# Optimization experiments

Measured on AMD Instinct MI355X. Metric: run time of the kernel, lower is better.

The kernel has to match this reference:

```python
import jax, jax.numpy as jnp
import numpy as np

N_NODES = 100_000
N_EDGES = 1_200_000
N_GRAPHS = 512
HID = 64


def setup_inputs() -> dict:
    key = jax.random.key(0)
    ks = jax.random.split(key, 8)
    x = jax.random.normal(ks[0], (N_NODES, 2), dtype=jnp.float32)
    edge_index = jax.random.randint(ks[1], (2, N_EDGES), 0, N_NODES, dtype=jnp.int32)
    batch = jnp.sort(jax.random.randint(ks[2], (N_NODES,), 0, N_GRAPHS, dtype=jnp.int32))
    def glorot(k, shape):
        fan_in, fan_out = shape
        s = jnp.sqrt(6.0 / (fan_in + fan_out))
        return jax.random.uniform(k, shape, jnp.float32, -s, s)
    return {
        "x": x, "edge_index": edge_index, "batch": batch, "num_graphs": N_GRAPHS,
        "W1": glorot(ks[3], (2, HID)), "b1": jnp.zeros((HID,), jnp.float32),
        "W2": glorot(ks[4], (HID, HID)), "b2": jnp.zeros((HID,), jnp.float32),
        "Wf1": glorot(ks[5], (HID, HID)), "bf1": jnp.zeros((HID,), jnp.float32),
        "Wf2": glorot(ks[6], (HID, 4)), "bf2": jnp.zeros((4,), jnp.float32),
    }


def gcn_conv(x, W, b, src, dst, n_nodes):
    """PyG GCNConv: sym-normalized A with self-loops, then linear."""
    h = x @ W  # [N, H] transform first (as PyG does)
    ones = jnp.ones(src.shape[0], x.dtype)
    deg = jax.ops.segment_sum(ones, dst, num_segments=n_nodes) + 1.0  # +1 self-loop
    dinv = jax.lax.rsqrt(deg)  # deg >= 1 always
    norm = dinv[src] * dinv[dst]  # [E]
    agg = jax.ops.segment_sum(h[src] * norm[:, None], dst, num_segments=n_nodes)
    agg = agg + h * (dinv * dinv)[:, None]  # self-loop contribution
    return agg + b


def global_mean_pool(x, batch, num_graphs):
    sums = jax.ops.segment_sum(x, batch, num_segments=num_graphs)
    cnts = jax.ops.segment_sum(jnp.ones(x.shape[0], x.dtype), batch, num_segments=num_graphs)
    return sums / jnp.maximum(cnts, 1.0)[:, None]


def reference(x, edge_index, batch, num_graphs, W1, b1, W2, b2, Wf1, bf1, Wf2, bf2):
    n = x.shape[0]
    src, dst = edge_index[0], edge_index[1]
    h = jax.nn.relu(gcn_conv(x, W1, b1, src, dst, n))   # dropout = identity (eval)
    h = jax.nn.relu(gcn_conv(h, W2, b2, src, dst, n))
    g = global_mean_pool(h, batch, num_graphs)          # [num_graphs, HID]
    g = jax.nn.relu(g @ Wf1 + bf1)
    return g @ Wf2 + bf2                                # [num_graphs, 4]
```

## Files before the change

### kernel.cpp

```cpp
#include <hip/hip_runtime.h>
#include <hip/hip_fp16.h>

#define NG 512
#define HID 64
#define CSH 9
#define BKT (1 << CSH)
#define PTILE 4096
#define MAXB 1024

__device__ __forceinline__ int pad8(int d) { return (d + 7) & ~7; }

__global__ __launch_bounds__(256) void partA_kernel(
    const int* __restrict__ src, const int* __restrict__ dst,
    const int* __restrict__ batch, int* __restrict__ gstart,
    int* __restrict__ bcnt, int* __restrict__ pstage,
    int E, int N, int nbc, int S) {
    __shared__ int hist[MAXB];
    __shared__ int base[MAXB];
    int tid = threadIdx.x;
    int t0 = blockIdx.x * PTILE;
    for (int i = blockIdx.x * 256 + tid; i < N; i += gridDim.x * 256) {
        int b = batch[i];
        int bp = (i == 0) ? -1 : batch[i - 1];
        for (int g = bp + 1; g <= b; ++g) gstart[g] = i;
        if (i == N - 1)
            for (int g = b + 1; g <= NG; ++g) gstart[g] = N;
    }
    for (int i = tid; i < nbc; i += 256) hist[i] = 0;
    __syncthreads();
    int es[PTILE / 256], ds[PTILE / 256];
#pragma unroll
    for (int j = 0; j < PTILE / 256; ++j) {
        int e = t0 + j * 256 + tid;
        if (e < E) {
            ds[j] = dst[e];
            es[j] = src[e];
            atomicAdd(&hist[ds[j] >> CSH], 1);
        } else {
            ds[j] = -1;
        }
    }
    __syncthreads();
    for (int i = tid; i < nbc; i += 256) {
        int c = hist[i];
        base[i] = c ? atomicAdd(&bcnt[i], c) : 0;
        hist[i] = 0;
    }
    __syncthreads();
#pragma unroll
    for (int j = 0; j < PTILE / 256; ++j) {
        if (ds[j] >= 0) {
            int b = ds[j] >> CSH;
            int r = base[b] + atomicAdd(&hist[b], 1);
            if (r < S)
                pstage[(size_t)b * S + r] = (es[j] << CSH) | (ds[j] & (BKT - 1));
        }
    }
}

__global__ __launch_bounds__(256) void partB2_kernel(
    const int* __restrict__ pstage, const int* __restrict__ bcnt,
    const float2* __restrict__ x2, int* __restrict__ deg, float* __restrict__ dinv,
    float2* __restrict__ xs2, int* __restrict__ rowbeg, int* __restrict__ esrc,
    int* __restrict__ ecur, int N, int S) {
    __shared__ int h[BKT];
    __shared__ int rowL[BKT];
    __shared__ int curL[BKT];
    __shared__ int ps[256];
    __shared__ int baseS;
    int c = blockIdx.x;
    int n0 = c << CSH;
    int tid = threadIdx.x;
    for (int i = tid; i < BKT; i += 256) h[i] = 0;
    __syncthreads();
    int cnt = min(bcnt[c], S);
    const int* pst = pstage + (size_t)c * S;
    for (int i = tid; i < cnt; i += 256) atomicAdd(&h[pst[i] & (BKT - 1)], 1);
    __syncthreads();
    int i0 = 2 * tid, i1 = 2 * tid + 1;
    int dg0 = (n0 + i0 < N) ? h[i0] : 0;
    int dg1 = (n0 + i1 < N) ? h[i1] : 0;
    if (n0 + i0 < N) {
        deg[n0 + i0] = dg0;
        float di = rsqrtf((float)dg0 + 1.0f);
        dinv[n0 + i0] = di;
        float2 xv = x2[n0 + i0];
        xs2[n0 + i0] = make_float2(xv.x * di, xv.y * di);
    }
    if (n0 + i1 < N) {
        deg[n0 + i1] = dg1;
        float di = rsqrtf((float)dg1 + 1.0f);
        dinv[n0 + i1] = di;
        float2 xv = x2[n0 + i1];
        xs2[n0 + i1] = make_float2(xv.x * di, xv.y * di);
    }
    int p0 = pad8(dg0), p1 = pad8(dg1);
    ps[tid] = p0 + p1;
    __syncthreads();
    for (int off = 1; off < 256; off <<= 1) {
        int t = (tid >= off) ? ps[tid - off] : 0;
        __syncthreads();
        ps[tid] += t;
        __syncthreads();
    }
    if (tid == 255) baseS = atomicAdd(ecur, ps[255]);
    __syncthreads();
    int excl = baseS + ps[tid] - (p0 + p1);
    rowL[i0] = excl;
    rowL[i1] = excl + p0;
    curL[i0] = 0;
    curL[i1] = 0;
    if (n0 + i0 < N) rowbeg[n0 + i0] = rowL[i0];
    if (n0 + i1 < N) rowbeg[n0 + i1] = rowL[i1];
    __syncthreads();
    for (int i = tid; i < cnt; i += 256) {
        int w = pst[i];
        int l = w & (BKT - 1);
        int p = rowL[l] + atomicAdd(&curL[l], 1);
        esrc[p] = w >> CSH;
    }
    __syncthreads();
    for (int l = tid; l < BKT; l += 256) {
        if (n0 + l < N) {
            int dg = curL[l];
            int p = rowL[l] + dg, p1e = rowL[l] + pad8(dg);
            for (; p < p1e; ++p) esrc[p] = N;
        }
    }
    if (c == 0 && tid == 0) xs2[N] = make_float2(0.0f, 0.0f);
}

__global__ __launch_bounds__(256) void layer1a_kernel(
    const float2* __restrict__ xs2, const int* __restrict__ rowbeg,
    const int* __restrict__ deg, const int* __restrict__ esrc,
    const float* __restrict__ dinv, const float* __restrict__ W1,
    const float* __restrict__ b1, float* __restrict__ h1s, int N) {
    int t = blockIdx.x * blockDim.x + threadIdx.x;
    int node = t >> 6, lane = t & 63;
    if (node >= N) return;
    int un = __builtin_amdgcn_readfirstlane(node);
    int k0 = __builtin_amdgcn_readfirstlane(rowbeg[un]);
    int k1 = k0 + pad8(__builtin_amdgcn_readfirstlane(deg[un]));
    float a0 = 0.0f, a1 = 0.0f;
    for (int e = k0; e < k1; e += 8) {
        const int4* ep = (const int4*)(esrc + e);
        int4 qa = ep[0], qb = ep[1];
        float2 v0 = xs2[qa.x], v1 = xs2[qa.y], v2 = xs2[qa.z], v3 = xs2[qa.w];
        float2 v4 = xs2[qb.x], v5 = xs2[qb.y], v6 = xs2[qb.z], v7 = xs2[qb.w];
        a0 += ((v0.x + v1.x) + (v2.x + v3.x)) + ((v4.x + v5.x) + (v6.x + v7.x));
        a1 += ((v0.y + v1.y) + (v2.y + v3.y)) + ((v4.y + v5.y) + (v6.y + v7.y));
    }
    float di = dinv[un];
    float2 xn = xs2[un];
    float m0 = di * (a0 + xn.x);
    float m1 = di * (a1 + xn.y);
    float v = fmaf(m0, W1[lane], fmaf(m1, W1[HID + lane], b1[lane]));
    h1s[(size_t)un * HID + lane] = fmaxf(v, 0.0f) * di;
}

#define TNB 128
__global__ __launch_bounds__(TNB) void l1gemm_kernel(
    const float* __restrict__ h1s, const float* __restrict__ W2,
    __half* __restrict__ h2, int N) {
    __shared__ float h1t[HID * TNB];
    int t = threadIdx.x;
    int node0 = blockIdx.x * TNB;
    const float4* g4 = (const float4*)h1s;
#pragma unroll
    for (int r = 0; r < 16; ++r) {
        int g = r * TNB + t;
        int nd = g >> 4, kq = g & 15;
        float4 v = make_float4(0.f, 0.f, 0.f, 0.f);
        if (node0 + nd < N) v = g4[(size_t)(node0 + nd) * 16 + kq];
        int kb = kq * 4;
        h1t[(kb + 0) * TNB + (nd ^ ((kb + 0) & 31))] = v.x;
        h1t[(kb + 1) * TNB + (nd ^ ((kb + 1) & 31))] = v.y;
        h1t[(kb + 2) * TNB + (nd ^ ((kb + 2) & 31))] = v.z;
        h1t[(kb + 3) * TNB + (nd ^ ((kb + 3) & 31))] = v.w;
    }
    __syncthreads();
    int node = node0 + t;
    bool alive = node < N;
#pragma unroll 1
    for (int jt = 0; jt < 8; ++jt) {
        float c0 = 0.f, c1 = 0.f, c2 = 0.f, c3 = 0.f;
        float c4 = 0.f, c5 = 0.f, c6 = 0.f, c7 = 0.f;
#pragma unroll 8
        for (int k = 0; k < HID; ++k) {
            float h = h1t[k * TNB + (t ^ (k & 31))];
            const float4* wr = (const float4*)(W2 + k * HID + jt * 8);
            float4 wa = wr[0], wb = wr[1];
            c0 = fmaf(h, wa.x, c0); c1 = fmaf(h, wa.y, c1);
            c2 = fmaf(h, wa.z, c2); c3 = fmaf(h, wa.w, c3);
            c4 = fmaf(h, wb.x, c4); c5 = fmaf(h, wb.y, c5);
            c6 = fmaf(h, wb.z, c6); c7 = fmaf(h, wb.w, c7);
        }
        if (alive) {
            union { __half h[8]; int4 v; } u;
            u.h[0] = __float2half_rn(c0); u.h[1] = __float2half_rn(c1);
            u.h[2] = __float2half_rn(c2); u.h[3] = __float2half_rn(c3);
            u.h[4] = __float2half_rn(c4); u.h[5] = __float2half_rn(c5);
            u.h[6] = __float2half_rn(c6); u.h[7] = __float2half_rn(c7);
            *(int4*)(h2 + (size_t)node * HID + jt * 8) = u.v;
        }
    }
}

__global__ __launch_bounds__(256, 8) void layer2_kernel(
    const int* __restrict__ rowbeg, const int* __restrict__ deg,
    const int* __restrict__ esrc, const float* __restrict__ dinv,
    const __half* __restrict__ h2, const float* __restrict__ b2,
    const int* __restrict__ batch, float* __restrict__ gsum, int N) {
    int lane = threadIdx.x & 63;
    float bz = b2[lane];
    int wave = (blockIdx.x * 256 + threadIdx.x) >> 6;
    int nwaves = gridDim.x * 4;
    int npw = (N + nwaves - 1) / nwaves;
    int nA = wave * npw;
    int nB = min(N, nA + npw);
    int gcur = -1;
    float zacc = 0.0f;
    for (int node = nA; node < nB; ++node) {
        int un = __builtin_amdgcn_readfirstlane(node);
        int k0 = __builtin_amdgcn_readfirstlane(rowbeg[un]);
        int k1 = k0 + pad8(__builtin_amdgcn_readfirstlane(deg[un]));
        float acc = __half2float(h2[(un << 6) + lane]);
        int e = k0;
        for (; e + 32 <= k1; e += 32) {
            const int4* ep = (const int4*)(esrc + e);
            int4 q0 = ep[0], q1 = ep[1], q2 = ep[2], q3 = ep[3];
            int4 q4 = ep[4], q5 = ep[5], q6 = ep[6], q7 = ep[7];
            float r0  = __half2float(h2[(q0.x << 6) + lane]);
            float r1  = __half2float(h2[(q0.y << 6) + lane]);
            float r2  = __half2float(h2[(q0.z << 6) + lane]);
            float r3  = __half2float(h2[(q0.w << 6) + lane]);
            float r4  = __half2float(h2[(q1.x << 6) + lane]);
            float r5  = __half2float(h2[(q1.y << 6) + lane]);
            float r6  = __half2float(h2[(q1.z << 6) + lane]);
            float r7  = __half2float(h2[(q1.w << 6) + lane]);
            float r8  = __half2float(h2[(q2.x << 6) + lane]);
            float r9  = __half2float(h2[(q2.y << 6) + lane]);
            float r10 = __half2float(h2[(q2.z << 6) + lane]);
            float r11 = __half2float(h2[(q2.w << 6) + lane]);
            float r12 = __half2float(h2[(q3.x << 6) + lane]);
            float r13 = __half2float(h2[(q3.y << 6) + lane]);
            float r14 = __half2float(h2[(q3.z << 6) + lane]);
            float r15 = __half2float(h2[(q3.w << 6) + lane]);
            float r16 = __half2float(h2[(q4.x << 6) + lane]);
            float r17 = __half2float(h2[(q4.y << 6) + lane]);
            float r18 = __half2float(h2[(q4.z << 6) + lane]);
            float r19 = __half2float(h2[(q4.w << 6) + lane]);
            float r20 = __half2float(h2[(q5.x << 6) + lane]);
            float r21 = __half2float(h2[(q5.y << 6) + lane]);
            float r22 = __half2float(h2[(q5.z << 6) + lane]);
            float r23 = __half2float(h2[(q5.w << 6) + lane]);
            float r24 = __half2float(h2[(q6.x << 6) + lane]);
            float r25 = __half2float(h2[(q6.y << 6) + lane]);
            float r26 = __half2float(h2[(q6.z << 6) + lane]);
            float r27 = __half2float(h2[(q6.w << 6) + lane]);
            float r28 = __half2float(h2[(q7.x << 6) + lane]);
            float r29 = __half2float(h2[(q7.y << 6) + lane]);
            float r30 = __half2float(h2[(q7.z << 6) + lane]);
            float r31 = __half2float(h2[(q7.w << 6) + lane]);
            acc += ((((r0 + r1) + (r2 + r3)) + ((r4 + r5) + (r6 + r7)))
                  + (((r8 + r9) + (r10 + r11)) + ((r12 + r13) + (r14 + r15))))
                 + ((((r16 + r17) + (r18 + r19)) + ((r20 + r21) + (r22 + r23)))
                  + (((r24 + r25) + (r26 + r27)) + ((r28 + r29) + (r30 + r31))));
        }
        if (e + 16 <= k1) {
            const int4* ep = (const int4*)(esrc + e);
            int4 qa = ep[0], qb = ep[1], qc = ep[2], qd = ep[3];
            float r0 = __half2float(h2[(qa.x << 6) + lane]);
            float r1 = __half2float(h2[(qa.y << 6) + lane]);
            float r2 = __half2float(h2[(qa.z << 6) + lane]);
            float r3 = __half2float(h2[(qa.w << 6) + lane]);
            float r4 = __half2float(h2[(qb.x << 6) + lane]);
            float r5 = __half2float(h2[(qb.y << 6) + lane]);
            float r6 = __half2float(h2[(qb.z << 6) + lane]);
            float r7 = __half2float(h2[(qb.w << 6) + lane]);
            float r8 = __half2float(h2[(qc.x << 6) + lane]);
            float r9 = __half2float(h2[(qc.y << 6) + lane]);
            float r10 = __half2float(h2[(qc.z << 6) + lane]);
            float r11 = __half2float(h2[(qc.w << 6) + lane]);
            float r12 = __half2float(h2[(qd.x << 6) + lane]);
            float r13 = __half2float(h2[(qd.y << 6) + lane]);
            float r14 = __half2float(h2[(qd.z << 6) + lane]);
            float r15 = __half2float(h2[(qd.w << 6) + lane]);
            acc += (((r0 + r1) + (r2 + r3)) + ((r4 + r5) + (r6 + r7)))
                 + (((r8 + r9) + (r10 + r11)) + ((r12 + r13) + (r14 + r15)));
            e += 16;
        }
        if (e < k1) {
            const int4* ep = (const int4*)(esrc + e);
            int4 qa = ep[0], qb = ep[1];
            float r0 = __half2float(h2[(qa.x << 6) + lane]);
            float r1 = __half2float(h2[(qa.y << 6) + lane]);
            float r2 = __half2float(h2[(qa.z << 6) + lane]);
            float r3 = __half2float(h2[(qa.w << 6) + lane]);
            float r4 = __half2float(h2[(qb.x << 6) + lane]);
            float r5 = __half2float(h2[(qb.y << 6) + lane]);
            float r6 = __half2float(h2[(qb.z << 6) + lane]);
            float r7 = __half2float(h2[(qb.w << 6) + lane]);
            acc += ((r0 + r1) + (r2 + r3)) + ((r4 + r5) + (r6 + r7));
        }
        float z = fmaxf(fmaf(dinv[un], acc, bz), 0.0f);
        int g = __builtin_amdgcn_readfirstlane(batch[un]);
        if (g != gcur) {
            if (gcur >= 0) atomicAdd(&gsum[(gcur << 6) + lane], zacc);
            gcur = g;
            zacc = 0.0f;
        }
        zacc += z;
    }
    if (gcur >= 0) atomicAdd(&gsum[(gcur << 6) + lane], zacc);
}

__global__ void head_kernel(const float* __restrict__ gsum, const int* __restrict__ gstart,
                            const float* __restrict__ Wf1, const float* __restrict__ bf1,
                            const float* __restrict__ Wf2, const float* __restrict__ bf2,
                            float* __restrict__ out) {
    __shared__ float gs[HID];
    __shared__ float ts[HID];
    int b = blockIdx.x;
    int j = threadIdx.x;
    float cnt = fmaxf((float)(gstart[b + 1] - gstart[b]), 1.0f);
    gs[j] = gsum[b * HID + j] / cnt;
    __syncthreads();
    float acc = bf1[j];
#pragma unroll
    for (int k = 0; k < HID; ++k) acc = fmaf(gs[k], Wf1[k * HID + j], acc);
    ts[j] = fmaxf(acc, 0.0f);
    __syncthreads();
    if (j < 4) {
        float o = bf2[j];
#pragma unroll
        for (int k = 0; k < HID; ++k) o = fmaf(ts[k], Wf2[k * 4 + j], o);
        out[b * 4 + j] = o;
    }
}

extern "C" void kernel_launch(void* const* d_in, const int* in_sizes, int n_in,
                              void* d_out, int out_size, void* d_ws, size_t ws_size,
                              hipStream_t stream) {
    const float* x   = (const float*)d_in[0];
    const int*   ei  = (const int*)d_in[1];
    const int*   bat = (const int*)d_in[2];
    const float* W1  = (const float*)d_in[4];
    const float* b1  = (const float*)d_in[5];
    const float* W2  = (const float*)d_in[6];
    const float* b2  = (const float*)d_in[7];
    const float* Wf1 = (const float*)d_in[8];
    const float* bf1 = (const float*)d_in[9];
    const float* Wf2 = (const float*)d_in[10];
    const float* bf2 = (const float*)d_in[11];
    float* out = (float*)d_out;

    int N = in_sizes[2];
    int E = in_sizes[1] / 2;
    const int* src = ei;
    const int* dst = ei + E;
    int nbc = (N + BKT - 1) >> CSH;
    int ntile = (E + PTILE - 1) / PTILE;
    int S = 2 * (E / nbc) + 1024;
    size_t Ecap = ((size_t)E + 7 * (size_t)N + 8 + 3) & ~(size_t)3;

    char* ws = (char*)d_ws;
    size_t off = 0;
    auto alloc = [&](size_t bytes) {
        char* p = ws + off;
        off = (off + bytes + 255) & ~(size_t)255;
        return p;
    };
    int*    bcnt   = (int*)alloc((size_t)MAXB * 4);
    int*    ecur   = (int*)alloc(256);
    float*  gsum   = (float*)alloc((size_t)NG * HID * 4);
    int*    deg    = (int*)alloc((size_t)N * 4);
    float*  dinv   = (float*)alloc((size_t)N * 4);
    int*    rowbeg = (int*)alloc((size_t)N * 4);
    int*    esrc   = (int*)alloc(Ecap * 4);
    int*    pstage = (int*)alloc((size_t)nbc * S * 4);
    float2* xs2    = (float2*)alloc((size_t)(N + 1) * 8);
    float*  h1buf  = (float*)alloc((size_t)N * HID * 4);
    __half* h2buf  = (__half*)alloc((size_t)(N + 1) * HID * 2);
    int*    gstart = (int*)alloc((size_t)(NG + 1) * 4);

    hipMemsetAsync(bcnt, 0, (size_t)((char*)gsum - (char*)bcnt) + (size_t)NG * HID * 4,
                   stream);
    hipMemsetAsync(h2buf + (size_t)N * HID, 0, HID * 2, stream);

    partA_kernel<<<ntile, 256, 0, stream>>>(src, dst, bat, gstart, bcnt, pstage, E, N,
                                            nbc, S);
    partB2_kernel<<<nbc, 256, 0, stream>>>(pstage, bcnt, (const float2*)x, deg, dinv, xs2,
                                           rowbeg, esrc, ecur, N, S);

    int nh = N * HID;
    layer1a_kernel<<<(nh + 255) / 256, 256, 0, stream>>>(xs2, rowbeg, deg, esrc, dinv, W1,
                                                         b1, h1buf, N);
    l1gemm_kernel<<<(N + TNB - 1) / TNB, TNB, 0, stream>>>(h1buf, W2, h2buf, N);

    layer2_kernel<<<4096, 256, 0, stream>>>(rowbeg, deg, esrc, dinv, h2buf, b2, bat, gsum,
                                            N);

    head_kernel<<<NG, HID, 0, stream>>>(gsum, gstart, Wf1, bf1, Wf2, bf2, out);
}
```

Measured before the change: 225.9 us.

## Fuse layer-1 aggregation with W2 GEMM via shared-memory tile, drop h1 buffer

Merges the layer-1 aggregation kernel and the 64x64 GEMM kernel into one. Each block aggregates 64 nodes, writes the scaled hidden vectors straight into a swizzled shared tile, then four waves each compute two output column groups. This removes the float32 h1 round trip through global memory (about 25 MB written and read back) and one kernel launch. The zeroing of the padding row moves from a memset into partB2. In exchange, GEMM parallelism changes, since each block handles fewer nodes and splits columns across waves, and the gather phase runs with one node per wave sequentially.

```diff
diff --git a/kernel.cpp b/kernel.cpp
--- a/kernel.cpp
+++ b/kernel.cpp
@@ -7,6 +7,7 @@
 #define BKT (1 << CSH)
 #define PTILE 4096
 #define MAXB 1024
+#define TNB 64
 
 __device__ __forceinline__ int pad8(int d) { return (d + 7) & ~7; }
 
@@ -62,7 +63,7 @@
     const int* __restrict__ pstage, const int* __restrict__ bcnt,
     const float2* __restrict__ x2, int* __restrict__ deg, float* __restrict__ dinv,
     float2* __restrict__ xs2, int* __restrict__ rowbeg, int* __restrict__ esrc,
-    int* __restrict__ ecur, int N, int S) {
+    int* __restrict__ ecur, __half* __restrict__ h2, int N, int S) {
     __shared__ int h[BKT];
     __shared__ int rowL[BKT];
     __shared__ int curL[BKT];
@@ -127,67 +128,60 @@
             for (; p < p1e; ++p) esrc[p] = N;
         }
     }
-    if (c == 0 && tid == 0) xs2[N] = make_float2(0.0f, 0.0f);
-}
-
-__global__ __launch_bounds__(256) void layer1a_kernel(
+    if (c == 0) {
+        if (tid == 0) xs2[N] = make_float2(0.0f, 0.0f);
+        if (tid < 8)
+            ((int4*)(h2 + (size_t)N * HID))[tid] = make_int4(0, 0, 0, 0);
+    }
+}
+
+__global__ __launch_bounds__(256) void layer1f_kernel(
     const float2* __restrict__ xs2, const int* __restrict__ rowbeg,
     const int* __restrict__ deg, const int* __restrict__ esrc,
     const float* __restrict__ dinv, const float* __restrict__ W1,
-    const float* __restrict__ b1, float* __restrict__ h1s, int N) {
-    int t = blockIdx.x * blockDim.x + threadIdx.x;
-    int node = t >> 6, lane = t & 63;
-    if (node >= N) return;
-    int un = __builtin_amdgcn_readfirstlane(node);
-    int k0 = __builtin_amdgcn_readfirstlane(rowbeg[un]);
-    int k1 = k0 + pad8(__builtin_amdgcn_readfirstlane(deg[un]));
-    float a0 = 0.0f, a1 = 0.0f;
-    for (int e = k0; e < k1; e += 8) {
-        const int4* ep = (const int4*)(esrc + e);
-        int4 qa = ep[0], qb = ep[1];
-        float2 v0 = xs2[qa.x], v1 = xs2[qa.y], v2 = xs2[qa.z], v3 = xs2[qa.w];
-        float2 v4 = xs2[qb.x], v5 = xs2[qb.y], v6 = xs2[qb.z], v7 = xs2[qb.w];
-        a0 += ((v0.x + v1.x) + (v2.x + v3.x)) + ((v4.x + v5.x) + (v6.x + v7.x));
-        a1 += ((v0.y + v1.y) + (v2.y + v3.y)) + ((v4.y + v5.y) + (v6.y + v7.y));
-    }
-    float di = dinv[un];
-    float2 xn = xs2[un];
-    float m0 = di * (a0 + xn.x);
-    float m1 = di * (a1 + xn.y);
-    float v = fmaf(m0, W1[lane], fmaf(m1, W1[HID + lane], b1[lane]));
-    h1s[(size_t)un * HID + lane] = fmaxf(v, 0.0f) * di;
-}
-
-#define TNB 128
-__global__ __launch_bounds__(TNB) void l1gemm_kernel(
-    const float* __restrict__ h1s, const float* __restrict__ W2,
+    const float* __restrict__ b1, const float* __restrict__ W2,
     __half* __restrict__ h2, int N) {
     __shared__ float h1t[HID * TNB];
-    int t = threadIdx.x;
+    int tid = threadIdx.x;
+    int lane = tid & 63;
+    int wv = tid >> 6;
     int node0 = blockIdx.x * TNB;
-    const float4* g4 = (const float4*)h1s;
-#pragma unroll
-    for (int r = 0; r < 16; ++r) {
-        int g = r * TNB + t;
-        int nd = g >> 4, kq = g & 15;
-        float4 v = make_float4(0.f, 0.f, 0.f, 0.f);
-        if (node0 + nd < N) v = g4[(size_t)(node0 + nd) * 16 + kq];
-        int kb = kq * 4;
-        h1t[(kb + 0) * TNB + (nd ^ ((kb + 0) & 31))] = v.x;
-        h1t[(kb + 1) * TNB + (nd ^ ((kb + 1) & 31))] = v.y;
-        h1t[(kb + 2) * TNB + (nd ^ ((kb + 2) & 31))] = v.z;
-        h1t[(kb + 3) * TNB + (nd ^ ((kb + 3) & 31))] = v.w;
-    }
-    __syncthreads();
-    int node = node0 + t;
+    for (int j = 0; j < TNB / 4; ++j) {
+        int nl = wv * (TNB / 4) + j;
+        int node = node0 + nl;
+        if (node < N) {
+            int un = __builtin_amdgcn_readfirstlane(node);
+            int k0 = __builtin_amdgcn_readfirstlane(rowbeg[un]);
+            int k1 = k0 + pad8(__builtin_amdgcn_readfirstlane(deg[un]));
+            float a0 = 0.0f, a1 = 0.0f;
+            for (int e = k0; e < k1; e += 8) {
+                const int4* ep = (const int4*)(esrc + e);
+                int4 qa = ep[0], qb = ep[1];
+                float2 v0 = xs2[qa.x], v1 = xs2[qa.y], v2 = xs2[qa.z], v3 = xs2[qa.w];
+                float2 v4 = xs2[qb.x], v5 = xs2[qb.y], v6 = xs2[qb.z], v7 = xs2[qb.w];
+                a0 += ((v0.x + v1.x) + (v2.x + v3.x)) + ((v4.x + v5.x) + (v6.x + v7.x));
+                a1 += ((v0.y + v1.y) + (v2.y + v3.y)) + ((v4.y + v5.y) + (v6.y + v7.y));
+            }
+            float di = dinv[un];
+            float2 xn = xs2[un];
+            float m0 = di * (a0 + xn.x);
+            float m1 = di * (a1 + xn.y);
+            float v = fmaf(m0, W1[lane], fmaf(m1, W1[HID + lane], b1[lane]));
+            h1t[lane * TNB + (nl ^ (lane & 31))] = fmaxf(v, 0.0f) * di;
+        }
+    }
+    __syncthreads();
+    int nd = tid & 63;
+    int node = node0 + nd;
     bool alive = node < N;
-#pragma unroll 1
-    for (int jt = 0; jt < 8; ++jt) {
+    int jb = wv * 2;
+#pragma unroll
+    for (int jt = jb; jt < jb + 2; ++jt) {
         float c0 = 0.f, c1 = 0.f, c2 = 0.f, c3 = 0.f;
         float c4 = 0.f, c5 = 0.f, c6 = 0.f, c7 = 0.f;
 #pragma unroll 8
         for (int k = 0; k < HID; ++k) {
-            float h = h1t[k * TNB + (t ^ (k & 31))];
+            float h = h1t[k * TNB + (nd ^ (k & 31))];
             const float4* wr = (const float4*)(W2 + k * HID + jt * 8);
             float4 wa = wr[0], wb = wr[1];
             c0 = fmaf(h, wa.x, c0); c1 = fmaf(h, wa.y, c1);
@@ -380,23 +374,19 @@
     int*    esrc   = (int*)alloc(Ecap * 4);
     int*    pstage = (int*)alloc((size_t)nbc * S * 4);
     float2* xs2    = (float2*)alloc((size_t)(N + 1) * 8);
-    float*  h1buf  = (float*)alloc((size_t)N * HID * 4);
     __half* h2buf  = (__half*)alloc((size_t)(N + 1) * HID * 2);
     int*    gstart = (int*)alloc((size_t)(NG + 1) * 4);
 
     hipMemsetAsync(bcnt, 0, (size_t)((char*)gsum - (char*)bcnt) + (size_t)NG * HID * 4,
                    stream);
-    hipMemsetAsync(h2buf + (size_t)N * HID, 0, HID * 2, stream);
 
     partA_kernel<<<ntile, 256, 0, stream>>>(src, dst, bat, gstart, bcnt, pstage, E, N,
                                             nbc, S);
     partB2_kernel<<<nbc, 256, 0, stream>>>(pstage, bcnt, (const float2*)x, deg, dinv, xs2,
-                                           rowbeg, esrc, ecur, N, S);
-
-    int nh = N * HID;
-    layer1a_kernel<<<(nh + 255) / 256, 256, 0, stream>>>(xs2, rowbeg, deg, esrc, dinv, W1,
-                                                         b1, h1buf, N);
-    l1gemm_kernel<<<(N + TNB - 1) / TNB, TNB, 0, stream>>>(h1buf, W2, h2buf, N);
+                                           rowbeg, esrc, ecur, h2buf, N, S);
+
+    layer1f_kernel<<<(N + TNB - 1) / TNB, 256, 0, stream>>>(xs2, rowbeg, deg, esrc, dinv,
+                                                            W1, b1, W2, h2buf, N);
 
     layer2_kernel<<<4096, 256, 0, stream>>>(rowbeg, deg, esrc, dinv, h2buf, b2, bat, gsum,
                                             N);
```

Measured after the change: 237.6 us. +5.2%, slower.
